# Kernel optimization log

Measured on AMD Instinct MI355X. Metric: run time of the kernel, lower is better.

## Reference

```python
import math
import jax, jax.numpy as jnp
import numpy as np

NUM_BUCKETS = 32
MAX_DISTANCE = 128
HEADS = 16
D_MODEL = 1024
SEQ = 1024
BATCH = 4
SCALE = (D_MODEL // HEADS) ** -0.5  # applied ONLY to the relative-position bias, per the source


def _rel_pos_bucket_causal(seq_len):
    """Causal T5 relative-position bucket: ret[i, j] for query i, key j."""
    pos = jnp.arange(seq_len)
    # rel_pos = k - q ; n = -rel_pos = q - k, clamped at 0 (causal branch)
    n = jnp.maximum(pos[:, None] - pos[None, :], 0)
    max_exact = NUM_BUCKETS // 2  # 16
    # log-spaced buckets for large distances; guard n>=1 to avoid log(0)
    val_large = max_exact + (
        jnp.log(jnp.maximum(n, 1).astype(jnp.float32) / max_exact)
        / math.log(MAX_DISTANCE / max_exact)
        * (NUM_BUCKETS - max_exact)
    ).astype(jnp.int32)
    val_large = jnp.minimum(val_large, NUM_BUCKETS - 1)
    return jnp.where(n < max_exact, n, val_large)  # [i, j] int32


def setup_inputs() -> dict:
    key = jax.random.key(0)
    ks = jax.random.split(key, 6)
    s = 0.02
    return {
        "x": jax.random.normal(ks[0], (BATCH, SEQ, D_MODEL), jnp.float32),
        "Wq": jax.random.normal(ks[1], (D_MODEL, D_MODEL), jnp.float32) * s,
        "bq": jnp.zeros((D_MODEL,), jnp.float32),
        "Wk": jax.random.normal(ks[2], (D_MODEL, D_MODEL), jnp.float32) * s,
        "bk": jnp.zeros((D_MODEL,), jnp.float32),
        "Wv": jax.random.normal(ks[3], (D_MODEL, D_MODEL), jnp.float32) * s,
        "bv": jnp.zeros((D_MODEL,), jnp.float32),
        "Wo": jax.random.normal(ks[4], (D_MODEL, D_MODEL), jnp.float32) * s,
        "bo": jnp.zeros((D_MODEL,), jnp.float32),
        "rel_emb": jax.random.normal(ks[5], (NUM_BUCKETS, HEADS), jnp.float32) * s,
    }


def reference(x, Wq, bq, Wk, bk, Wv, bv, Wo, bo, rel_emb):
    b, n, d = x.shape
    h, hd = HEADS, d // HEADS
    # projections (torch Linear: x @ W^T + b)
    q = (x @ Wq.T + bq).reshape(b, n, h, hd).transpose(0, 2, 1, 3)  # bhnd
    k = (x @ Wk.T + bk).reshape(b, n, h, hd).transpose(0, 2, 1, 3)
    v = (x @ Wv.T + bv).reshape(b, n, h, hd).transpose(0, 2, 1, 3)
    # unscaled dot-product scores (module does not scale q.k)
    sim = jnp.einsum("bhid,bhjd->bhij", q, k)
    # T5 relative-position bias, scaled by head_dim^-0.5
    rp_bucket = _rel_pos_bucket_causal(n)            # [i, j]
    bias = rel_emb[rp_bucket]                        # [i, j, h]
    sim = sim + jnp.transpose(bias, (2, 0, 1)) * SCALE  # broadcast over batch
    # additive causal mask (-inf above diagonal)
    i = jnp.arange(n)
    causal = jnp.where(i[None, :] > i[:, None], -jnp.inf, 0.0).astype(sim.dtype)
    sim = sim + causal
    attn = jax.nn.softmax(sim, axis=-1)
    out = jnp.einsum("bhij,bhjd->bhid", attn, v)
    out = out.transpose(0, 2, 1, 3).reshape(b, n, d)
    return out @ Wo.T + bo
```

## Files before the change

kernel.cpp:

```cpp
#include <hip/hip_runtime.h>
#include <hip/hip_bf16.h>
#include <stdint.h>

#define B_   4
#define SEQ_ 1024
#define DM   1024
#define H_   16
#define HD   64

typedef __bf16 bf16;
typedef __bf16 bf16x8 __attribute__((ext_vector_type(8)));
typedef __bf16 bf16x4v __attribute__((ext_vector_type(4)));
typedef __bf16 bf16x2 __attribute__((ext_vector_type(2)));
typedef float  f32x4 __attribute__((ext_vector_type(4)));

__device__ __forceinline__ void gl_lds16(const void* g, void* s_uniform) {
    __builtin_amdgcn_global_load_lds(
        (const __attribute__((address_space(1))) uint32_t*)g,
        (__attribute__((address_space(3))) uint32_t*)s_uniform,
        16, 0, 0);
}

__global__ __launch_bounds__(256) void prep_kernel(
    const float* __restrict__ x, const float* __restrict__ Wq,
    const float* __restrict__ Wk, const float* __restrict__ Wv,
    const float* __restrict__ Wo, const float* __restrict__ rel,
    bf16* __restrict__ xb, bf16* __restrict__ wqkvb, bf16* __restrict__ wob,
    float* __restrict__ biasT)
{
    int tid = blockIdx.x * 256 + threadIdx.x;
    int stride = gridDim.x * 256;

    for (int i = tid; i < (B_*SEQ_*DM)/4; i += stride) {
        float4 v = ((const float4*)x)[i];
        bf16x4v o; o[0]=(bf16)v.x; o[1]=(bf16)v.y; o[2]=(bf16)v.z; o[3]=(bf16)v.w;
        ((bf16x4v*)xb)[i] = o;
    }
    for (int i = tid; i < (3*DM*DM)/4; i += stride) {
        int n = i >> 8, k4 = i & 255;
        const float* src = (n < 1024) ? Wq : (n < 2048) ? Wk : Wv;
        float4 v = ((const float4*)(src + (size_t)(n & 1023) * DM))[k4];
        bf16x4v o; o[0]=(bf16)v.x; o[1]=(bf16)v.y; o[2]=(bf16)v.z; o[3]=(bf16)v.w;
        ((bf16x4v*)wqkvb)[i] = o;
    }
    for (int i = tid; i < (DM*DM)/4; i += stride) {
        float4 v = ((const float4*)Wo)[i];
        bf16x4v o; o[0]=(bf16)v.x; o[1]=(bf16)v.y; o[2]=(bf16)v.z; o[3]=(bf16)v.w;
        ((bf16x4v*)wob)[i] = o;
    }
    for (int i = tid; i < H_ * SEQ_; i += stride) {
        int h = i >> 10, dist = i & 1023;
        int bkt;
        if (dist < 16) {
            bkt = dist;
        } else {
            float r = logf((float)dist * (1.0f/16.0f)) / logf(8.0f) * 16.0f;
            int vb = 16 + (int)r;
            bkt = vb > 31 ? 31 : vb;
        }
        biasT[i] = rel[bkt * H_ + h] * (0.125f * 1.4426950408889634f);
    }
}

template<int NT>
__global__ __launch_bounds__(512, 4) void gemm_ring2(
    const bf16* __restrict__ Ag, const bf16* __restrict__ Bg,
    bf16* __restrict__ qb, bf16* __restrict__ kb, bf16* __restrict__ vtb,
    const float* __restrict__ bq, const float* __restrict__ bk,
    const float* __restrict__ bv)
{
    __shared__ __align__(16) bf16 tile[3][384 * 32];

    const int t = threadIdx.x;
    const int lane = t & 63, w = t >> 6;
    const int wr = w >> 1, wc = w & 1;
    const int row_l = lane & 15;
    const int lg = lane >> 4;

    int xcd = blockIdx.x & 7;
    int idx = blockIdx.x >> 3;
    int sub = idx / 24, rem = idx % 24;
    int ty = (xcd >> 1) * 4 + rem / 6;
    int tx = (xcd & 1) * 12 + sub * 6 + rem % 6;
    const int m0 = ty * 256, n0 = tx * 128;

    f32x4 acc[4][4] = {};

    auto STAGE = [&](int buf, int kt) {
        bf16* dst = &tile[buf][0];
        #pragma unroll
        for (int i = 0; i < 3; ++i) {
            int e = i * 4096 + t * 8;
            int r = e >> 5;
            int csw = ((t & 3) ^ (r & 3)) << 3;
            const bf16* src = (r < 256)
                ? (Ag + (long)(m0 + r) * 1024 + kt * 32 + csw)
                : (Bg + (long)(n0 + r - 256) * 1024 + kt * 32 + csw);
            gl_lds16(src, dst + i * 4096 + w * 512);
        }
    };

    auto COMPUTE = [&](int buf) {
        const bf16* bp = &tile[buf][0];
        bf16x8 af[4], bfr[4];
        #pragma unroll
        for (int m = 0; m < 4; ++m) {
            int ra = wr * 64 + m * 16 + row_l;
            af[m] = *(const bf16x8*)&bp[ra * 32 + ((lg ^ (ra & 3)) << 3)];
        }
        #pragma unroll
        for (int n = 0; n < 4; ++n) {
            int rb = 256 + wc * 64 + n * 16 + row_l;
            bfr[n] = *(const bf16x8*)&bp[rb * 32 + ((lg ^ (rb & 3)) << 3)];
        }
        #pragma unroll
        for (int m = 0; m < 4; ++m)
            #pragma unroll
            for (int n = 0; n < 4; ++n)
                acc[m][n] = __builtin_amdgcn_mfma_f32_16x16x32_bf16(
                    af[m], bfr[n], acc[m][n], 0, 0, 0);
    };

    STAGE(0, 0); STAGE(1, 1);
    asm volatile("s_waitcnt vmcnt(3)" ::: "memory");
    __builtin_amdgcn_s_barrier();

    int cb = 0;
    for (int kt = 0; kt < NT; ++kt) {
        int sb = cb - 1; if (sb < 0) sb += 3;
        if (kt + 2 < NT) STAGE(sb, kt + 2);
        COMPUTE(cb);
        if (kt + 2 < NT) { asm volatile("s_waitcnt vmcnt(3)" ::: "memory"); }
        else             { asm volatile("s_waitcnt vmcnt(0)" ::: "memory"); }
        __builtin_amdgcn_s_barrier();
        cb = (cb + 1 == 3) ? 0 : cb + 1;
    }

    const int rbase = (lane >> 4) * 4;

    if (n0 < 2048) {
        #pragma unroll
        for (int m = 0; m < 4; ++m) {
            #pragma unroll
            for (int n = 0; n < 4; ++n) {
                #pragma unroll
                for (int g = 0; g < 4; ++g) {
                    int gm = m0 + wr * 64 + m * 16 + rbase + g;
                    int gn = n0 + wc * 64 + n * 16 + row_l;
                    int which = gn >> 10, nn = gn & 1023;
                    int h = nn >> 6, d = nn & 63;
                    int b = gm >> 10, s = gm & 1023;
                    float v = acc[m][n][g] + ((which == 0) ? bq[nn] : bk[nn]);
                    if (which == 0) v *= 1.4426950408889634f;
                    bf16 bv16 = (bf16)v;
                    if (which == 0)
                        qb[((long)(b*H_ + h)*SEQ_ + s)*HD + d] = bv16;
                    else
                        kb[((long)(b*H_ + h)*SEQ_ + s)*HD + d] = bv16;
                }
            }
        }
    } else {
        bf16* lt = &tile[0][0];
        #pragma unroll
        for (int m = 0; m < 4; ++m) {
            #pragma unroll
            for (int n = 0; n < 4; ++n) {
                int nl = wc * 64 + n * 16 + row_l;
                int mlb = wr * 64 + m * 16 + rbase;
                float bvv = bv[(n0 & 1023) + nl];
                #pragma unroll
                for (int g2 = 0; g2 < 2; ++g2) {
                    bf16x2 pk;
                    pk[0] = (bf16)(acc[m][n][2*g2]     + bvv);
                    pk[1] = (bf16)(acc[m][n][2*g2 + 1] + bvv);
                    int ml = mlb + 2 * g2;
                    int byte = nl * 512 + ((ml * 2) ^ ((nl & 15) << 4));
                    *(bf16x2*)((char*)lt + byte) = pk;
                }
            }
        }
        __syncthreads();
        {
            int nl = t >> 2, sc = t & 3;
            int nn = (n0 & 1023) + nl;
            int h = nn >> 6, d = nn & 63;
            int b = m0 >> 10, s0 = (m0 & 1023) + sc * 64;
            bf16* dst = vtb + ((long)(b*H_ + h)*HD + d)*SEQ_ + s0;
            #pragma unroll
            for (int i = 0; i < 8; ++i) {
                int byte = nl * 512 + ((sc * 128 + i * 16) ^ ((nl & 15) << 4));
                *(float4*)(dst + i * 8) = *(const float4*)((char*)lt + byte);
            }
        }
    }
}

template<int NT>
__global__ __launch_bounds__(256, 2) void gemm_ring_o(
    const bf16* __restrict__ Ag, const bf16* __restrict__ Bg,
    float* __restrict__ outp, const float* __restrict__ bo)
{
    __shared__ __align__(16) bf16 tile[3][192 * 32];

    const int t = threadIdx.x;
    const int lane = t & 63, w = t >> 6;
    const int wr = w >> 1, wc = w & 1;
    const int row_l = lane & 15;
    const int lg = lane >> 4;

    int xcd = blockIdx.x & 7;
    int idx = blockIdx.x >> 3;
    int ty = (xcd >> 1) * 8 + (idx >> 3);
    int tx = (xcd & 1) * 8 + (idx & 7);
    const int m0 = ty * 128, n0 = tx * 64;

    f32x4 acc[4][2] = {};

    auto STAGE = [&](int buf, int kt) {
        bf16* dst = &tile[buf][0];
        #pragma unroll
        for (int i = 0; i < 3; ++i) {
            int e = i * 2048 + t * 8;
            int r = e >> 5;
            int csw = ((t & 3) ^ (r & 3)) << 3;
            const bf16* src = (r < 128)
                ? (Ag + (long)(m0 + r) * 1024 + kt * 32 + csw)
                : (Bg + (long)(n0 + r - 128) * 1024 + kt * 32 + csw);
            gl_lds16(src, dst + i * 2048 + w * 512);
        }
    };

    auto COMPUTE = [&](int buf) {
        const bf16* bp = &tile[buf][0];
        bf16x8 af[4], bfr[2];
        #pragma unroll
        for (int m = 0; m < 4; ++m) {
            int ra = wr * 64 + m * 16 + row_l;
            af[m] = *(const bf16x8*)&bp[ra * 32 + ((lg ^ (ra & 3)) << 3)];
        }
        #pragma unroll
        for (int n = 0; n < 2; ++n) {
            int rb = 128 + wc * 32 + n * 16 + row_l;
            bfr[n] = *(const bf16x8*)&bp[rb * 32 + ((lg ^ (rb & 3)) << 3)];
        }
        #pragma unroll
        for (int m = 0; m < 4; ++m)
            #pragma unroll
            for (int n = 0; n < 2; ++n)
                acc[m][n] = __builtin_amdgcn_mfma_f32_16x16x32_bf16(
                    af[m], bfr[n], acc[m][n], 0, 0, 0);
    };

    STAGE(0, 0); STAGE(1, 1);
    asm volatile("s_waitcnt vmcnt(3)" ::: "memory");
    __builtin_amdgcn_s_barrier();

    int cb = 0;
    for (int kt = 0; kt < NT; ++kt) {
        int sb = cb - 1; if (sb < 0) sb += 3;
        if (kt + 2 < NT) STAGE(sb, kt + 2);
        COMPUTE(cb);
        if (kt + 2 < NT) { asm volatile("s_waitcnt vmcnt(3)" ::: "memory"); }
        else             { asm volatile("s_waitcnt vmcnt(0)" ::: "memory"); }
        __builtin_amdgcn_s_barrier();
        cb = (cb + 1 == 3) ? 0 : cb + 1;
    }

    const int rbase = (lane >> 4) * 4;
    #pragma unroll
    for (int m = 0; m < 4; ++m) {
        #pragma unroll
        for (int n = 0; n < 2; ++n) {
            #pragma unroll
            for (int g = 0; g < 4; ++g) {
                int gm = m0 + wr * 64 + m * 16 + rbase + g;
                int gn = n0 + wc * 32 + n * 16 + row_l;
                outp[(long)gm * DM + gn] = acc[m][n][g] + bo[gn];
            }
        }
    }
}

__global__ __launch_bounds__(512, 4) void attn_kernel(
    const bf16* __restrict__ Qb, const bf16* __restrict__ Kb,
    const bf16* __restrict__ Vtb, const float* __restrict__ biasT,
    bf16* __restrict__ AO)
{
    __shared__ __align__(16) bf16 Ks[3][64 * 64];
    __shared__ __align__(16) bf16 Vs[3][64 * 64];
    __shared__ __align__(16) bf16 Ps[8][16 * 64];
    __shared__ float biasS[SEQ_];

    int t = threadIdx.x;
    int lane = t & 63, w = t >> 6;

    int bid = blockIdx.x;
    int xcd = bid & 7;
    int rest = bid >> 3;
    int g = xcd * 8 + (rest & 7);
    int pe = rest >> 3;
    int p = (pe < 4) ? pe : 11 - pe;
    int qt_hi = 15 - p;
    int h = g & 15, b = g >> 4;

    int qtw = (w < 4) ? p : qt_hi;
    int row0 = qtw * 64 + (w & 3) * 16;

    int row_l = lane & 15;
    int ksl = (lane >> 4) * 8;
    int rbase = (lane >> 4) * 4;

    const bf16* Kbase = Kb + (long)g * SEQ_ * HD;
    const bf16* Vbase = Vtb + (long)g * HD * SEQ_;

    auto stageKV = [&](int jt) {
        int sl = jt % 3;
        int e = t * 8;
        int r = e >> 6;
        int csw = ((((e >> 3) & 7) ^ (r & 7)) << 3);
        gl_lds16(Kbase + (long)(jt * 64 + r) * HD + csw, &Ks[sl][0] + w * 512);
        gl_lds16(Vbase + (long)r * SEQ_ + jt * 64 + csw, &Vs[sl][0] + w * 512);
    };

    stageKV(0);
    stageKV(1);
    if (t < 256)
        ((float4*)biasS)[t] = ((const float4*)(biasT + (long)h * SEQ_))[t];

    const bf16* Qp = Qb + ((long)g * SEQ_ + row0) * HD;
    bf16x8 qf0 = *(const bf16x8*)&Qp[row_l * HD + ksl];
    bf16x8 qf1 = *(const bf16x8*)&Qp[row_l * HD + 32 + ksl];

    f32x4 oacc[4] = {};
    float lsum[4] = {0.f, 0.f, 0.f, 0.f};
    int ir[4];
    #pragma unroll
    for (int q = 0; q < 4; ++q) ir[q] = row0 + rbase + q;

    __syncthreads();

    char* psw = (char*)&Ps[w][0];
    int prswz = (row_l & 7) << 4;

    for (int jt = 0; jt <= qt_hi; ++jt) {
        if (jt < qt_hi) { asm volatile("s_waitcnt vmcnt(2)" ::: "memory"); }
        else            { asm volatile("s_waitcnt vmcnt(0)" ::: "memory"); }
        __builtin_amdgcn_s_barrier();
        if (jt + 2 <= qt_hi) stageKV(jt + 2);

        if (jt <= qtw) {
            int sl = jt % 3;
            const bf16* kb_ = &Ks[sl][0];
            const bf16* vb_ = &Vs[sl][0];

            f32x4 s[4] = {};
            __builtin_amdgcn_s_setprio(1);
            #pragma unroll
            for (int f = 0; f < 4; ++f) {
                int ra = f * 16 + row_l;
                int a0 = (ra * 64 + ksl)      ^ ((ra & 7) << 3);
                int a1 = (ra * 64 + 32 + ksl) ^ ((ra & 7) << 3);
                bf16x8 kf0 = *(const bf16x8*)&kb_[a0];
                bf16x8 kf1 = *(const bf16x8*)&kb_[a1];
                s[f] = __builtin_amdgcn_mfma_f32_16x16x32_bf16(qf0, kf0, s[f], 0,0,0);
                s[f] = __builtin_amdgcn_mfma_f32_16x16x32_bf16(qf1, kf1, s[f], 0,0,0);
            }
            __builtin_amdgcn_s_setprio(0);

            if (jt < qtw) {
                #pragma unroll
                for (int f = 0; f < 4; ++f) {
                    int j = jt * 64 + f * 16 + row_l;
                    #pragma unroll
                    for (int q = 0; q < 4; ++q) {
                        float sv = s[f][q] + biasS[ir[q] - j];
                        float pexp = exp2f(sv);
                        lsum[q] += pexp;
                        int pr = rbase + q;
                        int byte = pr * 128 + ((((f*16 + row_l) * 2)) ^ ((pr & 7) << 4));
                        *(bf16*)(psw + byte) = (bf16)pexp;
                    }
                }
            } else {
                #pragma unroll
                for (int f = 0; f < 4; ++f) {
                    int j = jt * 64 + f * 16 + row_l;
                    #pragma unroll
                    for (int q = 0; q < 4; ++q) {
                        float sv = (j <= ir[q]) ? (s[f][q] + biasS[ir[q] - j]) : -1e30f;
                        float pexp = exp2f(sv);
                        lsum[q] += pexp;
                        int pr = rbase + q;
                        int byte = pr * 128 + ((((f*16 + row_l) * 2)) ^ ((pr & 7) << 4));
                        *(bf16*)(psw + byte) = (bf16)pexp;
                    }
                }
            }
            bf16x8 pf0 = *(const bf16x8*)(psw + row_l * 128 + ((ksl * 2) ^ prswz));
            bf16x8 pf1 = *(const bf16x8*)(psw + row_l * 128 + ((64 + ksl * 2) ^ prswz));

            __builtin_amdgcn_s_setprio(1);
            #pragma unroll
            for (int db = 0; db < 4; ++db) {
                int ra = db * 16 + row_l;
                int a0 = (ra * 64 + ksl)      ^ ((ra & 7) << 3);
                int a1 = (ra * 64 + 32 + ksl) ^ ((ra & 7) << 3);
                bf16x8 vf0 = *(const bf16x8*)&vb_[a0];
                bf16x8 vf1 = *(const bf16x8*)&vb_[a1];
                oacc[db] = __builtin_amdgcn_mfma_f32_16x16x32_bf16(pf0, vf0, oacc[db], 0,0,0);
                oacc[db] = __builtin_amdgcn_mfma_f32_16x16x32_bf16(pf1, vf1, oacc[db], 0,0,0);
            }
            __builtin_amdgcn_s_setprio(0);
        }
    }

    #pragma unroll
    for (int q = 0; q < 4; ++q) {
        float l = lsum[q];
        #pragma unroll
        for (int off = 1; off < 16; off <<= 1) l += __shfl_xor(l, off);
        float inv = 1.0f / l;
        long base = ((long)(b * SEQ_ + ir[q])) * DM + h * HD;
        #pragma unroll
        for (int db = 0; db < 4; ++db)
            AO[base + db * 16 + row_l] = (bf16)(oacc[db][q] * inv);
    }
}

extern "C" void kernel_launch(void* const* d_in, const int* in_sizes, int n_in,
                              void* d_out, int out_size, void* d_ws, size_t ws_size,
                              hipStream_t stream)
{
    const float* x   = (const float*)d_in[0];
    const float* Wq  = (const float*)d_in[1];
    const float* bq  = (const float*)d_in[2];
    const float* Wk  = (const float*)d_in[3];
    const float* bk  = (const float*)d_in[4];
    const float* Wv  = (const float*)d_in[5];
    const float* bv  = (const float*)d_in[6];
    const float* Wo  = (const float*)d_in[7];
    const float* bo  = (const float*)d_in[8];
    const float* rel = (const float*)d_in[9];
    float* out = (float*)d_out;

    char* ws = (char*)d_ws;
    bf16* xb    = (bf16*)ws;  ws += (size_t)B_*SEQ_*DM * 2;
    bf16* wqkvb = (bf16*)ws;  ws += (size_t)3*DM*DM * 2;
    bf16* wob   = (bf16*)ws;  ws += (size_t)DM*DM * 2;
    float* biasT= (float*)ws; ws += (size_t)H_*SEQ_ * 4;
    bf16* Qb    = (bf16*)ws;  ws += (size_t)B_*H_*SEQ_*HD * 2;
    bf16* Kb2   = (bf16*)ws;  ws += (size_t)B_*H_*SEQ_*HD * 2;
    bf16* Vtb   = (bf16*)ws;  ws += (size_t)B_*H_*SEQ_*HD * 2;
    bf16* AO    = (bf16*)ws;  ws += (size_t)B_*SEQ_*DM * 2;

    prep_kernel<<<2048, 256, 0, stream>>>(x, Wq, Wk, Wv, Wo, rel,
                                          xb, wqkvb, wob, biasT);

    gemm_ring2<32><<<384, 512, 0, stream>>>(
        xb, wqkvb, Qb, Kb2, Vtb, bq, bk, bv);

    attn_kernel<<<512, 512, 0, stream>>>(Qb, Kb2, Vtb, biasT, AO);

    gemm_ring_o<32><<<512, 256, 0, stream>>>(AO, wob, out, bo);
}
```

Measured before the change: 93.26 us.

## Enlarge QKV GEMM tiles to 256x256 with K=64 staged pipeline

Replaces the QKV projection GEMM's 256x128 tile with a 256x256 tile, K-step 64, 8 waves in a 2x4 layout and 8x4 accumulators per wave. Global-to-LDS loads are split into half-tiles interleaved with MFMA sub-steps, and s_setprio is raised around the MFMA bursts. The aim is more data reuse per byte loaded and better overlap of loads with compute. The cost is 128KB of LDS and more accumulator registers, which allow fewer resident blocks, and only 192 blocks, which may underfill the 256 CUs.

Result: no change. 92.47 us (-0.8%).

```diff
diff --git a/kernel.cpp b/kernel.cpp
--- a/kernel.cpp
+++ b/kernel.cpp
@@ -63,89 +63,121 @@
 }
 
 template<int NT>
-__global__ __launch_bounds__(512, 4) void gemm_ring2(
+__global__ __launch_bounds__(512, 2) void gemm8q(
     const bf16* __restrict__ Ag, const bf16* __restrict__ Bg,
     bf16* __restrict__ qb, bf16* __restrict__ kb, bf16* __restrict__ vtb,
     const float* __restrict__ bq, const float* __restrict__ bk,
     const float* __restrict__ bv)
 {
-    __shared__ __align__(16) bf16 tile[3][384 * 32];
+    __shared__ __align__(16) bf16 sh[65536];
+    bf16* As = sh;
+    bf16* Bs = sh + 32768;
 
     const int t = threadIdx.x;
     const int lane = t & 63, w = t >> 6;
-    const int wr = w >> 1, wc = w & 1;
+    const int wr = w >> 2, wc = w & 3;
     const int row_l = lane & 15;
     const int lg = lane >> 4;
 
     int xcd = blockIdx.x & 7;
     int idx = blockIdx.x >> 3;
-    int sub = idx / 24, rem = idx % 24;
-    int ty = (xcd >> 1) * 4 + rem / 6;
-    int tx = (xcd & 1) * 12 + sub * 6 + rem % 6;
-    const int m0 = ty * 256, n0 = tx * 128;
-
-    f32x4 acc[4][4] = {};
-
-    auto STAGE = [&](int buf, int kt) {
-        bf16* dst = &tile[buf][0];
-        #pragma unroll
-        for (int i = 0; i < 3; ++i) {
-            int e = i * 4096 + t * 8;
-            int r = e >> 5;
-            int csw = ((t & 3) ^ (r & 3)) << 3;
-            const bf16* src = (r < 256)
-                ? (Ag + (long)(m0 + r) * 1024 + kt * 32 + csw)
-                : (Bg + (long)(n0 + r - 256) * 1024 + kt * 32 + csw);
-            gl_lds16(src, dst + i * 4096 + w * 512);
+    int sub = idx / 12, rem = idx % 12;
+    int ty = (xcd >> 1) * 4 + rem / 3;
+    int tx = (xcd & 1) * 6 + sub * 3 + rem % 3;
+    const int m0 = ty * 256, n0 = tx * 256;
+
+    f32x4 acc[8][4] = {};
+
+    auto stageH = [&](bf16* lbase, const bf16* gbase, int grow0, int kt) {
+        #pragma unroll
+        for (int j = 0; j < 2; ++j) {
+            int rl = j * 64 + (t >> 3);
+            int csw = ((t & 7) ^ (rl & 7)) << 3;
+            gl_lds16(gbase + (long)(grow0 + rl) * 1024 + kt * 64 + csw,
+                     lbase + j * 4096 + w * 512);
         }
     };
 
-    auto COMPUTE = [&](int buf) {
-        const bf16* bp = &tile[buf][0];
-        bf16x8 af[4], bfr[4];
-        #pragma unroll
-        for (int m = 0; m < 4; ++m) {
-            int ra = wr * 64 + m * 16 + row_l;
-            af[m] = *(const bf16x8*)&bp[ra * 32 + ((lg ^ (ra & 3)) << 3)];
-        }
-        #pragma unroll
-        for (int n = 0; n < 4; ++n) {
-            int rb = 256 + wc * 64 + n * 16 + row_l;
-            bfr[n] = *(const bf16x8*)&bp[rb * 32 + ((lg ^ (rb & 3)) << 3)];
-        }
-        #pragma unroll
-        for (int m = 0; m < 4; ++m)
-            #pragma unroll
-            for (int n = 0; n < 4; ++n)
-                acc[m][n] = __builtin_amdgcn_mfma_f32_16x16x32_bf16(
-                    af[m], bfr[n], acc[m][n], 0, 0, 0);
-    };
-
-    STAGE(0, 0); STAGE(1, 1);
-    asm volatile("s_waitcnt vmcnt(3)" ::: "memory");
+    stageH(As,               Ag, m0,        0);
+    stageH(As + 8192,        Ag, m0 + 128,  0);
+    stageH(Bs,               Bg, n0,        0);
+    stageH(Bs + 8192,        Bg, n0 + 128,  0);
+    stageH(Bs + 16384,       Bg, n0,        1);
+    stageH(Bs + 16384 + 8192,Bg, n0 + 128,  1);
+    asm volatile("s_waitcnt vmcnt(4)" ::: "memory");
     __builtin_amdgcn_s_barrier();
 
-    int cb = 0;
-    for (int kt = 0; kt < NT; ++kt) {
-        int sb = cb - 1; if (sb < 0) sb += 3;
-        if (kt + 2 < NT) STAGE(sb, kt + 2);
-        COMPUTE(cb);
-        if (kt + 2 < NT) { asm volatile("s_waitcnt vmcnt(3)" ::: "memory"); }
-        else             { asm volatile("s_waitcnt vmcnt(0)" ::: "memory"); }
-        __builtin_amdgcn_s_barrier();
-        cb = (cb + 1 == 3) ? 0 : cb + 1;
+    for (int i = 0; i < NT/2; ++i) {
+        const bool more = (i + 1 < NT/2);
+        #pragma unroll
+        for (int ht = 0; ht < 2; ++ht) {
+            const bf16* Ad = As + (ht ? 16384 : 0);
+            const bf16* Bd = Bs + (ht ? 16384 : 0);
+            bf16x8 bfv[4][2];
+            #pragma unroll
+            for (int mh = 0; mh < 4; ++mh) {
+                bf16x8 afr[2][2];
+                if (mh == 0) {
+                    #pragma unroll
+                    for (int n = 0; n < 4; ++n)
+                        #pragma unroll
+                        for (int ks = 0; ks < 2; ++ks) {
+                            int rb = wc * 64 + n * 16 + row_l;
+                            int ch = ks * 4 + lg;
+                            bfv[n][ks] = *(const bf16x8*)&Bd[rb * 64 + ((ch ^ (rb & 7)) << 3)];
+                        }
+                }
+                #pragma unroll
+                for (int mm = 0; mm < 2; ++mm)
+                    #pragma unroll
+                    for (int ks = 0; ks < 2; ++ks) {
+                        int ra = wr * 128 + mh * 32 + mm * 16 + row_l;
+                        int ch = ks * 4 + lg;
+                        afr[mm][ks] = *(const bf16x8*)&Ad[ra * 64 + ((ch ^ (ra & 7)) << 3)];
+                    }
+
+                int p = ht * 4 + mh;
+                if (p == 0)      stageH(As + 16384,        Ag, m0,       2*i+1);
+                else if (p == 1) stageH(As + 16384 + 8192, Ag, m0 + 128, 2*i+1);
+                else if (more) {
+                    if (p == 2)      stageH(Bs,               Bg, n0,       2*i+2);
+                    else if (p == 3) stageH(Bs + 8192,        Bg, n0 + 128, 2*i+2);
+                    else if (p == 4) stageH(As,               Ag, m0,       2*i+2);
+                    else if (p == 5) stageH(As + 8192,        Ag, m0 + 128, 2*i+2);
+                    else if (p == 6) stageH(Bs + 16384,       Bg, n0,       2*i+3);
+                    else             stageH(Bs + 16384 + 8192,Bg, n0 + 128, 2*i+3);
+                }
+
+                __builtin_amdgcn_s_barrier();
+                __builtin_amdgcn_s_setprio(1);
+                #pragma unroll
+                for (int mm = 0; mm < 2; ++mm)
+                    #pragma unroll
+                    for (int n = 0; n < 4; ++n)
+                        #pragma unroll
+                        for (int ks = 0; ks < 2; ++ks)
+                            acc[mh*2+mm][n] = __builtin_amdgcn_mfma_f32_16x16x32_bf16(
+                                afr[mm][ks], bfv[n][ks], acc[mh*2+mm][n], 0, 0, 0);
+                __builtin_amdgcn_s_setprio(0);
+                if (p == 3 || p == 7) {
+                    if (more) { asm volatile("s_waitcnt vmcnt(4)" ::: "memory"); }
+                    else      { asm volatile("s_waitcnt vmcnt(0)" ::: "memory"); }
+                }
+                __builtin_amdgcn_s_barrier();
+            }
+        }
     }
 
     const int rbase = (lane >> 4) * 4;
 
     if (n0 < 2048) {
         #pragma unroll
-        for (int m = 0; m < 4; ++m) {
+        for (int m = 0; m < 8; ++m) {
             #pragma unroll
             for (int n = 0; n < 4; ++n) {
                 #pragma unroll
                 for (int g = 0; g < 4; ++g) {
-                    int gm = m0 + wr * 64 + m * 16 + rbase + g;
+                    int gm = m0 + wr * 128 + m * 16 + rbase + g;
                     int gn = n0 + wc * 64 + n * 16 + row_l;
                     int which = gn >> 10, nn = gn & 1023;
                     int h = nn >> 6, d = nn & 63;
@@ -161,36 +193,37 @@
             }
         }
     } else {
-        bf16* lt = &tile[0][0];
-        #pragma unroll
-        for (int m = 0; m < 4; ++m) {
+        __builtin_amdgcn_s_barrier();
+        #pragma unroll
+        for (int m = 0; m < 8; ++m) {
             #pragma unroll
             for (int n = 0; n < 4; ++n) {
-                int nl = wc * 64 + n * 16 + row_l;
-                int mlb = wr * 64 + m * 16 + rbase;
-                float bvv = bv[(n0 & 1023) + nl];
+                int col = wc * 64 + n * 16 + row_l;
+                int mlb = wr * 128 + m * 16 + rbase;
+                float bvv = bv[(n0 & 1023) + col];
                 #pragma unroll
                 for (int g2 = 0; g2 < 2; ++g2) {
                     bf16x2 pk;
                     pk[0] = (bf16)(acc[m][n][2*g2]     + bvv);
                     pk[1] = (bf16)(acc[m][n][2*g2 + 1] + bvv);
-                    int ml = mlb + 2 * g2;
-                    int byte = nl * 512 + ((ml * 2) ^ ((nl & 15) << 4));
-                    *(bf16x2*)((char*)lt + byte) = pk;
+                    int row = mlb + 2 * g2;
+                    int byte = col * 512 + ((row * 2) ^ ((col & 15) << 4));
+                    *(bf16x2*)((char*)sh + byte) = pk;
                 }
             }
         }
         __syncthreads();
         {
-            int nl = t >> 2, sc = t & 3;
-            int nn = (n0 & 1023) + nl;
+            int cr = t >> 1, sc = t & 1;
+            int nn = (n0 & 1023) + cr;
             int h = nn >> 6, d = nn & 63;
-            int b = m0 >> 10, s0 = (m0 & 1023) + sc * 64;
-            bf16* dst = vtb + ((long)(b*H_ + h)*HD + d)*SEQ_ + s0;
-            #pragma unroll
-            for (int i = 0; i < 8; ++i) {
-                int byte = nl * 512 + ((sc * 128 + i * 16) ^ ((nl & 15) << 4));
-                *(float4*)(dst + i * 8) = *(const float4*)((char*)lt + byte);
+            int b = m0 >> 10;
+            bf16* dst = vtb + ((long)(b*H_ + h)*HD + d)*SEQ_ + (m0 & 1023);
+            #pragma unroll
+            for (int ii = 0; ii < 16; ++ii) {
+                int chunk = sc * 16 + ii;
+                int byte = cr * 512 + ((chunk * 16) ^ ((cr & 15) << 4));
+                *(float4*)(dst + chunk * 8) = *(const float4*)((char*)sh + byte);
             }
         }
     }
@@ -457,7 +490,7 @@
     prep_kernel<<<2048, 256, 0, stream>>>(x, Wq, Wk, Wv, Wo, rel,
                                           xb, wqkvb, wob, biasT);
 
-    gemm_ring2<32><<<384, 512, 0, stream>>>(
+    gemm8q<16><<<192, 512, 0, stream>>>(
         xb, wqkvb, Qb, Kb2, Vtb, bq, bk, bv);
 
     attn_kernel<<<512, 512, 0, stream>>>(Qb, Kb2, Vtb, biasT, AO);
```
